# Optimization experiments

Hardware: AMD Instinct MI355X
Metric: run time of the kernel (lower is better)

The kernel has to match this reference:

```python
import jax, jax.numpy as jnp
import numpy as np

EPS = 1e-5

def _fake_quant(w, axis):
    # symmetric int8 fake-quant with straight-through estimator
    s = jnp.max(jnp.abs(w), axis=axis, keepdims=True) / 127.0 + 1e-8
    q = jnp.clip(jnp.round(w / s), -127.0, 127.0) * s
    return w + jax.lax.stop_gradient(q - w)

def _qconv1x1(x, w, b):
    # x: [B, C_in, Q, H, W]; w: [C_out, C_in] (1x1 kernel); weight fake-quantized
    wq = _fake_quant(w, axis=1)
    return jnp.einsum('bcqhw,oc->boqhw', x, wq) + b[None, :, None, None, None]

def setup_inputs() -> dict:
    key = jax.random.key(0)
    ks = jax.random.split(key, 12)
    B, C, Q, H, W = 8, 256, 4, 40, 40
    x = jax.random.normal(ks[0], (B, C, Q, H, W), dtype=jnp.float32)
    scale = 1.0 / np.sqrt(C)
    Wq = jax.random.normal(ks[1], (C, C), dtype=jnp.float32) * scale
    Wk = jax.random.normal(ks[2], (C, C), dtype=jnp.float32) * scale
    Wv = jax.random.normal(ks[3], (C, C), dtype=jnp.float32) * scale
    Wp = jax.random.normal(ks[4], (C, C), dtype=jnp.float32) * scale
    bq = jnp.zeros((C,), jnp.float32)
    bk = jnp.zeros((C,), jnp.float32)
    bv = jnp.zeros((C,), jnp.float32)
    bp = jnp.zeros((C,), jnp.float32)
    gamma = jnp.ones((C,), jnp.float32)
    beta = jnp.zeros((C,), jnp.float32)
    return {"x": x, "Wq": Wq, "bq": bq, "Wk": Wk, "bk": bk,
            "Wv": Wv, "bv": bv, "Wp": Wp, "bp": bp,
            "gamma": gamma, "beta": beta}

def reference(x, Wq, bq, Wk, bk, Wv, bv, Wp, bp, gamma, beta):
    B, C, Q, H, W = x.shape
    q = _qconv1x1(x, Wq, bq)
    k = _qconv1x1(x, Wk, bk)
    v = _qconv1x1(x, Wv, bv)
    # per-rotation channel attention: [B, Q=4, C, H*W]
    qh = q.reshape(B, C, Q, H * W).transpose(0, 2, 1, 3)
    kh = k.reshape(B, C, Q, H * W).transpose(0, 2, 1, 3)
    vh = v.reshape(B, C, Q, H * W).transpose(0, 2, 1, 3)
    scale = 1.0 / jnp.sqrt(jnp.float32(C // 4))
    attn = jnp.einsum('bqcn,bqdn->bqcd', qh, kh) * scale  # [B,4,C,C]
    attn = jax.nn.softmax(attn, axis=-1)
    out = jnp.einsum('bqcd,bqdn->bqcn', attn, vh)  # [B,4,C,HW]
    out = out.transpose(0, 2, 1, 3).reshape(B, C, Q, H, W)
    out = _qconv1x1(out, Wp, bp)
    # IQBN: per-channel batchnorm with int8 fake-quantized gamma
    mean = jnp.mean(out, axis=(0, 2, 3, 4), keepdims=True)
    var = jnp.var(out, axis=(0, 2, 3, 4), keepdims=True)
    g = _fake_quant(gamma, axis=None)[None, :, None, None, None]
    b = beta[None, :, None, None, None]
    out = (out - mean) * jax.lax.rsqrt(var + EPS) * g + b
    return out
```

## Files before the change

kernel.cpp:

```cpp
#include <hip/hip_runtime.h>
#include <math.h>

#define BB 8
#define CCH 256
#define QQ 4
#define NN 1600
#define BQN 32
#define SP 51200
#define EPSF 1e-5f

typedef __attribute__((ext_vector_type(8))) short bf16x8;
typedef __attribute__((ext_vector_type(4))) float f32x4;

static __device__ inline ushort f2bf(float f) {
  union { float f; unsigned u; } v; v.f = f;
  return (ushort)((v.u + 0x7fffu + ((v.u >> 16) & 1u)) >> 16);
}
static __device__ inline float bf2f(ushort u) {
  union { unsigned u; float f; } v; v.u = ((unsigned)u) << 16;
  return v.f;
}
static __device__ inline void gld16(const ushort* g, ushort* l) {
  __builtin_amdgcn_global_load_lds(
      (const __attribute__((address_space(1))) unsigned int*)g,
      (__attribute__((address_space(3))) unsigned int*)l, 16, 0, 0);
}

__global__ void quant_weights_kernel(const float* Wq, const float* Wk,
                                     const float* Wv, const float* Wp,
                                     const float* gamma,
                                     ushort* wq, ushort* wk, ushort* wvT, ushort* wp,
                                     ushort* wqT, ushort* wkT, ushort* wpT,
                                     float* gq, float* r, float* d2,
                                     float* m_acc, float* v_acc) {
  __shared__ float red[256];
  int blk = blockIdx.x;
  int tid = threadIdx.x;
  if (blk < 1024) {
    int mat = blk >> 8;
    int row = blk & 255;
    const float* W = (mat == 0) ? Wq : (mat == 1) ? Wk : (mat == 2) ? Wv : Wp;
    float w = W[row * 256 + tid];
    red[tid] = fabsf(w);
    __syncthreads();
    for (int s = 128; s > 0; s >>= 1) {
      if (tid < s) red[tid] = fmaxf(red[tid], red[tid + s]);
      __syncthreads();
    }
    float s = red[0] / 127.0f + 1e-8f;
    float q = fminf(fmaxf(rintf(w / s), -127.0f), 127.0f) * s;
    ushort qb = f2bf(q);
    if (mat == 0)      { wq[row * 256 + tid] = qb; wqT[tid * 256 + row] = qb; }
    else if (mat == 1) { wk[row * 256 + tid] = qb; wkT[tid * 256 + row] = qb; }
    else if (mat == 2) { wvT[tid * 256 + row] = qb; }
    else               { wp[row * 256 + tid] = qb; wpT[tid * 256 + row] = qb; }
  } else {
    float g = gamma[tid];
    red[tid] = fabsf(g);
    __syncthreads();
    for (int s = 128; s > 0; s >>= 1) {
      if (tid < s) red[tid] = fmaxf(red[tid], red[tid + s]);
      __syncthreads();
    }
    float s = red[0] / 127.0f + 1e-8f;
    gq[tid] = fminf(fmaxf(rintf(g / s), -127.0f), 127.0f) * s;
    for (int i = tid; i < BQN * 256; i += 256) { r[i] = 0.f; d2[i] = 0.f; }
    m_acc[tid] = 0.f;
    v_acc[tid] = 0.f;
  }
}

__global__ __launch_bounds__(256)
void prep_kernel(const float* __restrict__ x, ushort* __restrict__ xb,
                 ushort* __restrict__ xT, float* __restrict__ r) {
  int bqi = blockIdx.z, b = bqi >> 2, q = bqi & 3;
  int s0 = blockIdx.x * 64, c0 = blockIdx.y * 64;
  __shared__ ushort lT[64 * 66];
  int tid = threadIdx.x;
  int c = tid >> 2, nch = (tid & 3) * 16;
  const float* xp = x + ((size_t)(b * CCH + c0 + c) * QQ + q) * NN + s0 + nch;
  union { ushort u[16]; int4 v[2]; } nb;
  float s = 0.f;
#pragma unroll
  for (int j = 0; j < 4; j++) {
    float4 f = ((const float4*)xp)[j];
    ushort b0 = f2bf(f.x), b1 = f2bf(f.y), b2 = f2bf(f.z), b3 = f2bf(f.w);
    s += bf2f(b0) + bf2f(b1) + bf2f(b2) + bf2f(b3);
    nb.u[j * 4 + 0] = b0;
    nb.u[j * 4 + 1] = b1;
    nb.u[j * 4 + 2] = b2;
    nb.u[j * 4 + 3] = b3;
    lT[c * 66 + nch + j * 4 + 0] = b0;
    lT[c * 66 + nch + j * 4 + 1] = b1;
    lT[c * 66 + nch + j * 4 + 2] = b2;
    lT[c * 66 + nch + j * 4 + 3] = b3;
  }
  ushort* xbp = xb + (size_t)bqi * (CCH * NN) + (size_t)(c0 + c) * NN + s0 + nch;
  *(int4*)xbp = nb.v[0];
  *((int4*)xbp + 1) = nb.v[1];
  s += __shfl_down(s, 2);
  s += __shfl_down(s, 1);
  if ((tid & 3) == 0) atomicAdd(&r[bqi * 256 + c0 + c], s);
  __syncthreads();
  int n = tid >> 2, cch = (tid & 3) * 16;
  union { ushort u[16]; int4 v[2]; } o;
#pragma unroll
  for (int i = 0; i < 16; i++) o.u[i] = lT[(cch + i) * 66 + n];
  ushort* dst = xT + (size_t)(bqi * NN + s0 + n) * CCH + c0 + cch;
  *(int4*)dst = o.v[0];
  *((int4*)dst + 1) = o.v[1];
}

__global__ __launch_bounds__(256)
void gram_kernel(const ushort* __restrict__ xb, ushort* __restrict__ Gh,
                 ushort* __restrict__ Gl) {
  __shared__ __align__(16) char smem[32768];
  float* lC = (float*)smem;
  int z = blockIdx.z;
  int mBase = blockIdx.y * 128, nBase = blockIdx.x * 128;
  int tid = threadIdx.x, wave = tid >> 6, lane = tid & 63;
  int wm = wave >> 1, wn = wave & 1;
  int col = lane & 15, quad = lane >> 4;
  int srow = tid >> 2, skc = (tid & 3) * 8;
  const ushort* X = xb + (size_t)z * (CCH * NN);
  const ushort* gA  = X + (size_t)(mBase + srow) * NN + skc;
  const ushort* gA2 = gA + (size_t)64 * NN;
  const ushort* gB  = X + (size_t)(nBase + srow) * NN + skc;
  const ushort* gB2 = gB + (size_t)64 * NN;
  ushort* sA1[2]; ushort* sA2[2]; ushort* sB1[2]; ushort* sB2[2];
#pragma unroll
  for (int b = 0; b < 2; b++) {
    ushort* lAb = (ushort*)(smem + b * 16384);
    ushort* lBb = (ushort*)(smem + b * 16384 + 8192);
    sA1[b] = &lAb[srow * 32 + skc];
    sA2[b] = &lAb[(64 + srow) * 32 + skc];
    sB1[b] = &lBb[srow * 32 + skc];
    sB2[b] = &lBb[(64 + srow) * 32 + skc];
  }
  f32x4 acc[4][4];
#pragma unroll
  for (int i = 0; i < 4; i++)
#pragma unroll
    for (int j = 0; j < 4; j++) acc[i][j] = (f32x4){0.f, 0.f, 0.f, 0.f};

  const int nIter = NN / 32;
  gld16(gA, sA1[0]); gld16(gA2, sA2[0]); gld16(gB, sB1[0]); gld16(gB2, sB2[0]);
  for (int it = 0; it < nIter; ++it) {
    int cur = it & 1;
    __syncthreads();
    if (it + 1 < nIter) {
      int kt = (it + 1) << 5, nxt = cur ^ 1;
      gld16(gA + kt, sA1[nxt]); gld16(gA2 + kt, sA2[nxt]);
      gld16(gB + kt, sB1[nxt]); gld16(gB2 + kt, sB2[nxt]);
    }
    const ushort* lAc = (const ushort*)(smem + cur * 16384);
    const ushort* lBc = (const ushort*)(smem + cur * 16384 + 8192);
    bf16x8 af[4], bfr[4];
#pragma unroll
    for (int i = 0; i < 4; i++)
      af[i] = *(const bf16x8*)&lAc[(wm * 64 + i * 16 + col) * 32 + quad * 8];
#pragma unroll
    for (int j = 0; j < 4; j++)
      bfr[j] = *(const bf16x8*)&lBc[(wn * 64 + j * 16 + col) * 32 + quad * 8];
#pragma unroll
    for (int i = 0; i < 4; i++)
#pragma unroll
      for (int j = 0; j < 4; j++)
        acc[i][j] = __builtin_amdgcn_mfma_f32_16x16x32_bf16(af[i], bfr[j], acc[i][j], 0, 0, 0);
  }
  __syncthreads();
  float* lCw = lC + wave * 16 * 68;
  int mW = mBase + wm * 64, nW = nBase + wn * 64;
#pragma unroll
  for (int i = 0; i < 4; i++) {
#pragma unroll
    for (int j = 0; j < 4; j++)
#pragma unroll
      for (int rg = 0; rg < 4; rg++)
        lCw[(quad * 4 + rg) * 68 + j * 16 + col] = acc[i][j][rg];
    int mrow0 = mW + i * 16;
    int rr = lane & 15, cc = lane >> 4;
    union { ushort u[16]; int4 v[2]; } oh, ol;
#pragma unroll
    for (int t = 0; t < 16; t++) {
      float vfl = lCw[rr * 68 + cc * 16 + t];
      ushort hh = f2bf(vfl);
      oh.u[t] = hh;
      ol.u[t] = f2bf(vfl - bf2f(hh));
    }
    size_t off = (size_t)z * 65536 + (size_t)(mrow0 + rr) * 256 + nW + cc * 16;
    *(int4*)(Gh + off) = oh.v[0];
    *((int4*)(Gh + off) + 1) = oh.v[1];
    *(int4*)(Gl + off) = ol.v[0];
    *((int4*)(Gl + off) + 1) = ol.v[1];
  }
}

template<int MODE>
__global__ __launch_bounds__(256)
void gemm64(const ushort* __restrict__ A, long sA, const ushort* __restrict__ A2,
            const ushort* __restrict__ B, long sB, const ushort* __restrict__ B2,
            void* __restrict__ C1, void* __restrict__ C2, long sC) {
  constexpr bool SPB = (MODE == 0 || MODE == 4);
  constexpr bool SPA = (MODE == 1);
  constexpr int BUFB = (SPA || SPB) ? 12288 : 8192;
  __shared__ __align__(16) char smem[2 * BUFB];
  int z = blockIdx.z;
  int mBase = blockIdx.y * 64, nBase = blockIdx.x * 64;
  int tid = threadIdx.x, wave = tid >> 6, lane = tid & 63;
  int wm = wave >> 1, wn = wave & 1;
  int col = lane & 15, quad = lane >> 4;
  const ushort* gA = A + (size_t)z * sA + (size_t)(mBase + (tid >> 2)) * 256 + (tid & 3) * 8;
  const ushort* gB = B + (size_t)z * sB + (size_t)(nBase + (tid >> 2)) * 256 + (tid & 3) * 8;
  const ushort* gX = nullptr;
  if (SPB) gX = B2 + (size_t)z * sB + (size_t)(nBase + (tid >> 2)) * 256 + (tid & 3) * 8;
  if (SPA) gX = A2 + (size_t)z * sA + (size_t)(mBase + (tid >> 2)) * 256 + (tid & 3) * 8;

  f32x4 acc[2][2];
#pragma unroll
  for (int i = 0; i < 2; i++)
#pragma unroll
    for (int j = 0; j < 2; j++) acc[i][j] = (f32x4){0.f, 0.f, 0.f, 0.f};

  {
    char* bb = smem;
    gld16(gA, (ushort*)bb + tid * 8);
    gld16(gB, (ushort*)(bb + 4096) + tid * 8);
    if (SPA || SPB) gld16(gX, (ushort*)(bb + 8192) + tid * 8);
  }
  for (int it = 0; it < 8; ++it) {
    int cur = it & 1;
    __syncthreads();
    if (it + 1 < 8) {
      int kt = (it + 1) * 32;
      char* bb = smem + (cur ^ 1) * BUFB;
      gld16(gA + kt, (ushort*)bb + tid * 8);
      gld16(gB + kt, (ushort*)(bb + 4096) + tid * 8);
      if (SPA || SPB) gld16(gX + kt, (ushort*)(bb + 8192) + tid * 8);
    }
    const ushort* lA = (const ushort*)(smem + cur * BUFB);
    const ushort* lB = lA + 2048;
    const ushort* lX = lA + 4096;
    bf16x8 af[2], bfv[2], xf[2];
#pragma unroll
    for (int i = 0; i < 2; i++)
      af[i] = *(const bf16x8*)&lA[(wm * 32 + i * 16 + col) * 32 + quad * 8];
#pragma unroll
    for (int j = 0; j < 2; j++)
      bfv[j] = *(const bf16x8*)&lB[(wn * 32 + j * 16 + col) * 32 + quad * 8];
    if (SPB) {
#pragma unroll
      for (int j = 0; j < 2; j++)
        xf[j] = *(const bf16x8*)&lX[(wn * 32 + j * 16 + col) * 32 + quad * 8];
    } else if (SPA) {
#pragma unroll
      for (int i = 0; i < 2; i++)
        xf[i] = *(const bf16x8*)&lX[(wm * 32 + i * 16 + col) * 32 + quad * 8];
    }
#pragma unroll
    for (int i = 0; i < 2; i++)
#pragma unroll
      for (int j = 0; j < 2; j++) {
        acc[i][j] = __builtin_amdgcn_mfma_f32_16x16x32_bf16(af[i], bfv[j], acc[i][j], 0, 0, 0);
        if (SPB)
          acc[i][j] = __builtin_amdgcn_mfma_f32_16x16x32_bf16(af[i], xf[j], acc[i][j], 0, 0, 0);
        if (SPA)
          acc[i][j] = __builtin_amdgcn_mfma_f32_16x16x32_bf16(xf[i], bfv[j], acc[i][j], 0, 0, 0);
      }
  }

  if (MODE == 4) {
    const ushort* Tz = A + (size_t)z * sA;
    float* d2 = (float*)C1;
#pragma unroll
    for (int i = 0; i < 2; i++) {
      int mr = mBase + wm * 32 + i * 16 + quad * 4;
#pragma unroll
      for (int rg = 0; rg < 4; rg++) {
        float p = 0.f;
#pragma unroll
        for (int j = 0; j < 2; j++)
          p += acc[i][j][rg] * bf2f(Tz[(mr + rg) * 256 + nBase + wn * 32 + j * 16 + col]);
        p += __shfl_down(p, 8);
        p += __shfl_down(p, 4);
        p += __shfl_down(p, 2);
        p += __shfl_down(p, 1);
        if (col == 0) atomicAdd(d2 + z * 256 + mr + rg, p);
      }
    }
    return;
  }

  __syncthreads();
  float* lCw = (float*)smem + wave * (16 * 36);
#pragma unroll
  for (int i = 0; i < 2; i++) {
#pragma unroll
    for (int j = 0; j < 2; j++)
#pragma unroll
      for (int rg = 0; rg < 4; rg++)
        lCw[(quad * 4 + rg) * 36 + j * 16 + col] = acc[i][j][rg];
    int mrow0 = mBase + wm * 32 + i * 16;
    int nW = nBase + wn * 32;
    if (MODE == 1) {
      int rr = lane >> 2, cc = (lane & 3) * 8;
      float* C = (float*)C1 + (size_t)z * sC + (size_t)(mrow0 + rr) * 256 + nW + cc;
      float4 f0, f1;
      f0.x = lCw[rr * 36 + cc + 0]; f0.y = lCw[rr * 36 + cc + 1];
      f0.z = lCw[rr * 36 + cc + 2]; f0.w = lCw[rr * 36 + cc + 3];
      f1.x = lCw[rr * 36 + cc + 4]; f1.y = lCw[rr * 36 + cc + 5];
      f1.z = lCw[rr * 36 + cc + 6]; f1.w = lCw[rr * 36 + cc + 7];
      *(float4*)C = f0;
      *(float4*)(C + 4) = f1;
    } else if (MODE == 0) {
      int rr = lane >> 2, cc = (lane & 3) * 8;
      union { ushort u[8]; int4 v; } oh, ol;
#pragma unroll
      for (int t = 0; t < 8; t++) {
        float vf = lCw[rr * 36 + cc + t];
        ushort hh = f2bf(vf);
        oh.u[t] = hh;
        ol.u[t] = f2bf(vf - bf2f(hh));
      }
      size_t off = (size_t)z * sC + (size_t)(mrow0 + rr) * 256 + nW + cc;
      *(int4*)((ushort*)C1 + off) = oh.v;
      *(int4*)((ushort*)C2 + off) = ol.v;
    } else {
      if (MODE == 3) {
        int rr = lane >> 2, cc = (lane & 3) * 8;
        union { ushort u[8]; int4 v; } o;
#pragma unroll
        for (int t = 0; t < 8; t++) o.u[t] = f2bf(lCw[rr * 36 + cc + t]);
        *(int4*)((ushort*)C1 + (size_t)z * sC + (size_t)(mrow0 + rr) * 256 + nW + cc) = o.v;
      }
      int nn = lane >> 1, mh = (lane & 1) * 8;
      union { ushort u[8]; int4 v; } o2;
#pragma unroll
      for (int t = 0; t < 8; t++) o2.u[t] = f2bf(lCw[(mh + t) * 36 + nn]);
      ushort* CT = (ushort*)((MODE == 2) ? C1 : C2);
      *(int4*)(CT + (size_t)z * sC + (size_t)(nW + nn) * 256 + mrow0 + mh) = o2.v;
    }
  }
}

__global__ __launch_bounds__(256)
void uv_kernel(const ushort* __restrict__ wqT, const ushort* __restrict__ wkT,
               const float* __restrict__ r, float* __restrict__ u,
               float* __restrict__ vv) {
  int bq = blockIdx.x, sel = blockIdx.y, c = threadIdx.x;
  __shared__ float rs[256];
  rs[c] = r[bq * 256 + c];
  __syncthreads();
  const ushort* WT = sel ? wkT : wqT;
  float s = 0.f;
  for (int i = 0; i < 256; i++) s += bf2f(WT[i * 256 + c]) * rs[i];
  (sel ? vv : u)[bq * 256 + c] = s;
}

__global__ __launch_bounds__(256)
void softmax_kernel(const float* __restrict__ S, const float* __restrict__ u,
                    const float* __restrict__ vv, const float* __restrict__ bqv,
                    const float* __restrict__ bkv, const float* __restrict__ bvv,
                    ushort* __restrict__ P, float* __restrict__ pb) {
  int wave = threadIdx.x >> 6, lane = threadIdx.x & 63;
  int rglob = blockIdx.x * 4 + wave;
  int bq = rglob >> 8, rw = rglob & 255;
  size_t off = (size_t)rglob * 256;
  int c0 = lane * 4;
  float4 s4 = *(const float4*)(S + off + c0);
  float4 v4 = *(const float4*)(vv + bq * 256 + c0);
  float4 bk4 = *(const float4*)(bkv + c0);
  float4 bv4 = *(const float4*)(bvv + c0);
  float uu = u[bq * 256 + rw];
  float bqc = bqv[rw];
  float x0 = 0.125f * (s4.x + uu * bk4.x + bqc * v4.x + 1600.0f * bqc * bk4.x);
  float x1 = 0.125f * (s4.y + uu * bk4.y + bqc * v4.y + 1600.0f * bqc * bk4.y);
  float x2 = 0.125f * (s4.z + uu * bk4.z + bqc * v4.z + 1600.0f * bqc * bk4.z);
  float x3 = 0.125f * (s4.w + uu * bk4.w + bqc * v4.w + 1600.0f * bqc * bk4.w);
  float m = fmaxf(fmaxf(x0, x1), fmaxf(x2, x3));
#pragma unroll
  for (int s = 32; s > 0; s >>= 1) m = fmaxf(m, __shfl_xor(m, s));
  float e0 = expf(x0 - m), e1 = expf(x1 - m), e2 = expf(x2 - m), e3 = expf(x3 - m);
  float t = e0 + e1 + e2 + e3;
#pragma unroll
  for (int s = 32; s > 0; s >>= 1) t += __shfl_xor(t, s);
  float is = 1.0f / t;
  float p0 = e0 * is, p1 = e1 * is, p2 = e2 * is, p3 = e3 * is;
  union { ushort u[4]; uint2 v; } o;
  o.u[0] = f2bf(p0); o.u[1] = f2bf(p1); o.u[2] = f2bf(p2); o.u[3] = f2bf(p3);
  *(uint2*)(P + off + c0) = o.v;
  float d = p0 * bv4.x + p1 * bv4.y + p2 * bv4.z + p3 * bv4.w;
#pragma unroll
  for (int s = 32; s > 0; s >>= 1) d += __shfl_xor(d, s);
  if (lane == 0) pb[rglob] = d;
}

__global__ __launch_bounds__(256)
void bo_d1_kernel(const ushort* __restrict__ wpT, const ushort* __restrict__ TmT,
                  const float* __restrict__ pb, const float* __restrict__ rb,
                  const float* __restrict__ bp, const float* __restrict__ d2,
                  float* __restrict__ bo, float* __restrict__ m_acc,
                  float* __restrict__ v_acc) {
  int z = blockIdx.x, o = threadIdx.x;
  __shared__ float sp[256], sr[256];
  sp[o] = pb[z * 256 + o];
  sr[o] = rb[z * 256 + o];
  __syncthreads();
  float bv = bp[o], d1 = 0.f;
  const ushort* Tz = TmT + (size_t)z * 65536;
  for (int c = 0; c < 256; c++) {
    bv += bf2f(wpT[c * 256 + o]) * sp[c];
    d1 += bf2f(Tz[c * 256 + o]) * sr[c];
  }
  bo[z * 256 + o] = bv;
  atomicAdd(m_acc + o, d1 + 1600.0f * bv);
  atomicAdd(v_acc + o, d2[z * 256 + o] + 2.0f * bv * d1 + 1600.0f * bv * bv);
}

__global__ __launch_bounds__(256)
void final_kernel(const ushort* __restrict__ Tm, const ushort* __restrict__ xT,
                  const float* __restrict__ bo, const float* __restrict__ m_acc,
                  const float* __restrict__ v_acc, const float* __restrict__ gq,
                  const float* __restrict__ beta, float* __restrict__ out) {
  __shared__ __align__(16) char smem[32768];
  float* lC = (float*)smem;
  int z = blockIdx.z;
  int mBase = blockIdx.y * 128, nBase = blockIdx.x * 128;
  int tid = threadIdx.x, wave = tid >> 6, lane = tid & 63;
  int wm = wave >> 1, wn = wave & 1;
  int col = lane & 15, quad = lane >> 4;
  int srow = tid >> 2, skc = (tid & 3) * 8;
  const ushort* Az = Tm + (size_t)z * 65536;
  const ushort* Bz = xT + (size_t)z * (NN * 256);
  const ushort* gA  = Az + (size_t)(mBase + srow) * 256 + skc;
  const ushort* gA2 = gA + 64 * 256;
  int br1 = nBase + srow;      br1 = br1 < NN ? br1 : NN - 1;
  int br2 = nBase + 64 + srow; br2 = br2 < NN ? br2 : NN - 1;
  const ushort* gB  = Bz + (size_t)br1 * 256 + skc;
  const ushort* gB2 = Bz + (size_t)br2 * 256 + skc;
  ushort* sA1[2]; ushort* sA2[2]; ushort* sB1[2]; ushort* sB2[2];
#pragma unroll
  for (int b = 0; b < 2; b++) {
    ushort* lAb = (ushort*)(smem + b * 16384);
    ushort* lBb = (ushort*)(smem + b * 16384 + 8192);
    sA1[b] = &lAb[srow * 32 + skc];
    sA2[b] = &lAb[(64 + srow) * 32 + skc];
    sB1[b] = &lBb[srow * 32 + skc];
    sB2[b] = &lBb[(64 + srow) * 32 + skc];
  }
  f32x4 acc[4][4];
#pragma unroll
  for (int i = 0; i < 4; i++)
#pragma unroll
    for (int j = 0; j < 4; j++) acc[i][j] = (f32x4){0.f, 0.f, 0.f, 0.f};

  const int nIter = 8;
  gld16(gA, sA1[0]); gld16(gA2, sA2[0]); gld16(gB, sB1[0]); gld16(gB2, sB2[0]);
  for (int it = 0; it < nIter; ++it) {
    int cur = it & 1;
    __syncthreads();
    if (it + 1 < nIter) {
      int kt = (it + 1) << 5, nxt = cur ^ 1;
      gld16(gA + kt, sA1[nxt]); gld16(gA2 + kt, sA2[nxt]);
      gld16(gB + kt, sB1[nxt]); gld16(gB2 + kt, sB2[nxt]);
    }
    const ushort* lAc = (const ushort*)(smem + cur * 16384);
    const ushort* lBc = (const ushort*)(smem + cur * 16384 + 8192);
    bf16x8 af[4], bfr[4];
#pragma unroll
    for (int i = 0; i < 4; i++)
      af[i] = *(const bf16x8*)&lAc[(wm * 64 + i * 16 + col) * 32 + quad * 8];
#pragma unroll
    for (int j = 0; j < 4; j++)
      bfr[j] = *(const bf16x8*)&lBc[(wn * 64 + j * 16 + col) * 32 + quad * 8];
#pragma unroll
    for (int i = 0; i < 4; i++)
#pragma unroll
      for (int j = 0; j < 4; j++)
        acc[i][j] = __builtin_amdgcn_mfma_f32_16x16x32_bf16(af[i], bfr[j], acc[i][j], 0, 0, 0);
  }
  __syncthreads();
  float* lCw = lC + wave * 16 * 68;
  int mW = mBase + wm * 64, nW = nBase + wn * 64;
  int b = z >> 2, q = z & 3;
  const float inv = 1.0f / (float)SP;
#pragma unroll
  for (int i = 0; i < 4; i++) {
#pragma unroll
    for (int j = 0; j < 4; j++)
#pragma unroll
      for (int rg = 0; rg < 4; rg++)
        lCw[(quad * 4 + rg) * 68 + j * 16 + col] = acc[i][j][rg];
    int mrow0 = mW + i * 16;
    int rr = lane & 15, cc = lane >> 4;
    int n0 = nW + cc * 16;
    int o = mrow0 + rr;
    float bi = bo[(size_t)z * 256 + o];
    float mean = m_acc[o] * inv;
    float var = v_acc[o] * inv - mean * mean;
    float scl = rsqrtf(var + EPSF) * gq[o];
    float be = beta[o];
    if (n0 < NN) {
      float* C = out + (size_t)b * (CCH * QQ * NN)
               + (size_t)o * (QQ * NN) + (size_t)q * NN + n0;
#pragma unroll
      for (int v = 0; v < 4; v++) {
        float4 f;
        f.x = (lCw[rr * 68 + cc * 16 + v * 4 + 0] + bi - mean) * scl + be;
        f.y = (lCw[rr * 68 + cc * 16 + v * 4 + 1] + bi - mean) * scl + be;
        f.z = (lCw[rr * 68 + cc * 16 + v * 4 + 2] + bi - mean) * scl + be;
        f.w = (lCw[rr * 68 + cc * 16 + v * 4 + 3] + bi - mean) * scl + be;
        *(float4*)(C + v * 4) = f;
      }
    }
  }
}

extern "C" void kernel_launch(void* const* d_in, const int* in_sizes, int n_in,
                              void* d_out, int out_size, void* d_ws, size_t ws_size,
                              hipStream_t stream) {
  const float* x     = (const float*)d_in[0];
  const float* Wq    = (const float*)d_in[1];
  const float* bq    = (const float*)d_in[2];
  const float* Wk    = (const float*)d_in[3];
  const float* bk    = (const float*)d_in[4];
  const float* Wv    = (const float*)d_in[5];
  const float* bv    = (const float*)d_in[6];
  const float* Wp    = (const float*)d_in[7];
  const float* bp    = (const float*)d_in[8];
  const float* gamma = (const float*)d_in[9];
  const float* beta  = (const float*)d_in[10];
  float* out = (float*)d_out;

  ushort* h    = (ushort*)d_ws;
  ushort* wq   = h;
  ushort* wk   = wq + 65536;
  ushort* wp   = wk + 65536;
  ushort* wvT  = wp + 65536;
  ushort* wqT  = wvT + 65536;
  ushort* wkT  = wqT + 65536;
  ushort* wpT  = wkT + 65536;
  ushort* xb   = wpT + 65536;
  ushort* xT   = xb + (size_t)BQN * CCH * NN;
  ushort* Gh   = xT + (size_t)BQN * CCH * NN;
  ushort* Gl   = Gh + (size_t)BQN * 65536;
  ushort* M1h  = Gl + (size_t)BQN * 65536;
  ushort* M1l  = M1h + (size_t)BQN * 65536;
  ushort* P    = M1l + (size_t)BQN * 65536;
  ushort* N1t  = P + (size_t)BQN * 65536;
  ushort* Tm   = N1t + (size_t)BQN * 65536;
  ushort* TmT  = Tm + (size_t)BQN * 65536;
  float*  S    = (float*)(TmT + (size_t)BQN * 65536);
  float*  r    = S + (size_t)BQN * 65536;
  float*  u    = r + 8192;
  float*  vv   = u + 8192;
  float*  pb   = vv + 8192;
  float*  bo   = pb + 8192;
  float*  d2   = bo + 8192;
  float*  m_acc = d2 + 8192;
  float*  v_acc = m_acc + 256;
  float*  gq   = v_acc + 256;

  quant_weights_kernel<<<1025, 256, 0, stream>>>(Wq, Wk, Wv, Wp, gamma,
                                                 wq, wk, wvT, wp, wqT, wkT, wpT,
                                                 gq, r, d2, m_acc, v_acc);
  prep_kernel<<<dim3(NN / 64, CCH / 64, BQN), 256, 0, stream>>>(x, xb, xT, r);
  uv_kernel<<<dim3(BQN, 2), 256, 0, stream>>>(wqT, wkT, r, u, vv);
  gram_kernel<<<dim3(2, 2, BQN), 256, 0, stream>>>(xb, Gh, Gl);
  gemm64<0><<<dim3(4, 4, BQN), 256, 0, stream>>>(
      wq, 0, nullptr, Gh, 65536, Gl, M1h, M1l, 65536);
  gemm64<1><<<dim3(4, 4, BQN), 256, 0, stream>>>(
      M1h, 65536, M1l, wk, 0, nullptr, S, nullptr, 65536);
  softmax_kernel<<<BQN * CCH / 4, 256, 0, stream>>>(S, u, vv, bq, bk, bv, P, pb);
  gemm64<2><<<dim3(4, 4, BQN), 256, 0, stream>>>(
      P, 65536, nullptr, wvT, 0, nullptr, N1t, nullptr, 65536);
  gemm64<3><<<dim3(4, 4, BQN), 256, 0, stream>>>(
      wp, 0, nullptr, N1t, 65536, nullptr, Tm, TmT, 65536);
  gemm64<4><<<dim3(4, 4, BQN), 256, 0, stream>>>(
      Tm, 65536, nullptr, Gh, 65536, Gl, d2, nullptr, 0);
  bo_d1_kernel<<<BQN, 256, 0, stream>>>(wpT, TmT, pb, r, bp, d2, bo, m_acc, v_acc);
  final_kernel<<<dim3(13, 2, BQN), 256, 0, stream>>>(Tm, xT, bo, m_acc, v_acc,
                                                     gq, beta, out);
}
```

Measured before the change: 264.4 us.

## Exploit Gram symmetry and fuse attention GEMM chain into two kernels

The Gram kernel now computes only the upper-triangular 64x64 tiles (10 per batch-rotation) and writes mirrored transposes, roughly halving its MFMA work. The two M1/S GEMMs plus softmax are fused into one kernel that keeps M1 hi/lo in LDS, and the P·Wv and Wp GEMMs are fused into another that keeps N1 in LDS. This removes global round-trips for M1, S and N1 and several launches, but uses large LDS (about 100 KB) and fewer blocks (8 per z), which lowers occupancy and parallelism.

Measured after the change: 250.9 us. 1.05x faster.

```diff
diff --git a/kernel.cpp b/kernel.cpp
--- a/kernel.cpp
+++ b/kernel.cpp
@@ -112,87 +112,362 @@
 }
 
 __global__ __launch_bounds__(256)
-void gram_kernel(const ushort* __restrict__ xb, ushort* __restrict__ Gh,
-                 ushort* __restrict__ Gl) {
-  __shared__ __align__(16) char smem[32768];
-  float* lC = (float*)smem;
-  int z = blockIdx.z;
-  int mBase = blockIdx.y * 128, nBase = blockIdx.x * 128;
+void gram_sym_kernel(const ushort* __restrict__ xb, ushort* __restrict__ Gh,
+                     ushort* __restrict__ Gl) {
+  __shared__ __align__(16) char smem[16384];
+  int t = blockIdx.x, z = blockIdx.y;
+  int ty = (t >= 4) + (t >= 7) + (t >= 9);
+  int base = ty * 4 - (ty * (ty - 1)) / 2;
+  int tx = ty + (t - base);
+  int mBase = ty * 64, nBase = tx * 64;
+  bool offd = (tx != ty);
   int tid = threadIdx.x, wave = tid >> 6, lane = tid & 63;
   int wm = wave >> 1, wn = wave & 1;
   int col = lane & 15, quad = lane >> 4;
-  int srow = tid >> 2, skc = (tid & 3) * 8;
   const ushort* X = xb + (size_t)z * (CCH * NN);
-  const ushort* gA  = X + (size_t)(mBase + srow) * NN + skc;
-  const ushort* gA2 = gA + (size_t)64 * NN;
-  const ushort* gB  = X + (size_t)(nBase + srow) * NN + skc;
-  const ushort* gB2 = gB + (size_t)64 * NN;
-  ushort* sA1[2]; ushort* sA2[2]; ushort* sB1[2]; ushort* sB2[2];
-#pragma unroll
-  for (int b = 0; b < 2; b++) {
-    ushort* lAb = (ushort*)(smem + b * 16384);
-    ushort* lBb = (ushort*)(smem + b * 16384 + 8192);
-    sA1[b] = &lAb[srow * 32 + skc];
-    sA2[b] = &lAb[(64 + srow) * 32 + skc];
-    sB1[b] = &lBb[srow * 32 + skc];
-    sB2[b] = &lBb[(64 + srow) * 32 + skc];
-  }
-  f32x4 acc[4][4];
-#pragma unroll
-  for (int i = 0; i < 4; i++)
-#pragma unroll
-    for (int j = 0; j < 4; j++) acc[i][j] = (f32x4){0.f, 0.f, 0.f, 0.f};
+  const ushort* gA = X + (size_t)(mBase + (tid >> 2)) * NN + (tid & 3) * 8;
+  const ushort* gB = X + (size_t)(nBase + (tid >> 2)) * NN + (tid & 3) * 8;
+  f32x4 acc[2][2];
+#pragma unroll
+  for (int i = 0; i < 2; i++)
+#pragma unroll
+    for (int j = 0; j < 2; j++) acc[i][j] = (f32x4){0.f, 0.f, 0.f, 0.f};
 
   const int nIter = NN / 32;
-  gld16(gA, sA1[0]); gld16(gA2, sA2[0]); gld16(gB, sB1[0]); gld16(gB2, sB2[0]);
+  gld16(gA, (ushort*)smem + tid * 8);
+  gld16(gB, (ushort*)(smem + 4096) + tid * 8);
   for (int it = 0; it < nIter; ++it) {
     int cur = it & 1;
     __syncthreads();
     if (it + 1 < nIter) {
-      int kt = (it + 1) << 5, nxt = cur ^ 1;
-      gld16(gA + kt, sA1[nxt]); gld16(gA2 + kt, sA2[nxt]);
-      gld16(gB + kt, sB1[nxt]); gld16(gB2 + kt, sB2[nxt]);
-    }
-    const ushort* lAc = (const ushort*)(smem + cur * 16384);
-    const ushort* lBc = (const ushort*)(smem + cur * 16384 + 8192);
-    bf16x8 af[4], bfr[4];
+      int kt = (it + 1) << 5;
+      char* bb = smem + (cur ^ 1) * 8192;
+      gld16(gA + kt, (ushort*)bb + tid * 8);
+      gld16(gB + kt, (ushort*)(bb + 4096) + tid * 8);
+    }
+    const ushort* lA = (const ushort*)(smem + cur * 8192);
+    const ushort* lB = lA + 2048;
+    bf16x8 af[2], bfr[2];
+#pragma unroll
+    for (int i = 0; i < 2; i++)
+      af[i] = *(const bf16x8*)&lA[(wm * 32 + i * 16 + col) * 32 + quad * 8];
+#pragma unroll
+    for (int j = 0; j < 2; j++)
+      bfr[j] = *(const bf16x8*)&lB[(wn * 32 + j * 16 + col) * 32 + quad * 8];
+#pragma unroll
+    for (int i = 0; i < 2; i++)
+#pragma unroll
+      for (int j = 0; j < 2; j++)
+        acc[i][j] = __builtin_amdgcn_mfma_f32_16x16x32_bf16(af[i], bfr[j], acc[i][j], 0, 0, 0);
+  }
+  __syncthreads();
+  float* lCw = (float*)smem + wave * 576;
+#pragma unroll
+  for (int i = 0; i < 2; i++) {
+#pragma unroll
+    for (int j = 0; j < 2; j++)
+#pragma unroll
+      for (int rg = 0; rg < 4; rg++)
+        lCw[(quad * 4 + rg) * 36 + j * 16 + col] = acc[i][j][rg];
+    int mrow0 = mBase + wm * 32 + i * 16;
+    int nW = nBase + wn * 32;
+    int rr = lane >> 2, cc = (lane & 3) * 8;
+    union { ushort u[8]; int4 v; } oh, ol;
+#pragma unroll
+    for (int t8 = 0; t8 < 8; t8++) {
+      float vfl = lCw[rr * 36 + cc + t8];
+      ushort hh = f2bf(vfl);
+      oh.u[t8] = hh;
+      ol.u[t8] = f2bf(vfl - bf2f(hh));
+    }
+    size_t off = (size_t)z * 65536 + (size_t)(mrow0 + rr) * 256 + nW + cc;
+    *(int4*)(Gh + off) = oh.v;
+    *(int4*)(Gl + off) = ol.v;
+    if (offd) {
+      int nn = lane >> 1, mh = (lane & 1) * 8;
+      union { ushort u[8]; int4 v; } th, tl;
+#pragma unroll
+      for (int t8 = 0; t8 < 8; t8++) {
+        float vfl = lCw[(mh + t8) * 36 + nn];
+        ushort hh = f2bf(vfl);
+        th.u[t8] = hh;
+        tl.u[t8] = f2bf(vfl - bf2f(hh));
+      }
+      size_t offT = (size_t)z * 65536 + (size_t)(nW + nn) * 256 + mrow0 + mh;
+      *(int4*)(Gh + offT) = th.v;
+      *(int4*)(Gl + offT) = tl.v;
+    }
+  }
+}
+
+__global__ __launch_bounds__(256)
+void spk_kernel(const ushort* __restrict__ wq, const ushort* __restrict__ Gh,
+                const ushort* __restrict__ Gl, const ushort* __restrict__ wk,
+                const float* __restrict__ ug, const float* __restrict__ vg,
+                const float* __restrict__ bqv, const float* __restrict__ bkv,
+                const float* __restrict__ bvv,
+                ushort* __restrict__ P, float* __restrict__ pb) {
+  __shared__ __align__(16) char smem[103424];
+  int z = blockIdx.y, mBase = blockIdx.x * 32;
+  int tid = threadIdx.x, wave = tid >> 6, lane = tid & 63;
+  int col = lane & 15, quad = lane >> 4;
+  int rA = tid >> 2, sub = (tid & 3) * 8;
+  const ushort* Ghz = Gh + (size_t)z * 65536;
+  const ushort* Glz = Gl + (size_t)z * 65536;
+  ushort* M1h_l = (ushort*)(smem + 69632);
+  ushort* M1l_l = M1h_l + 8448;
+
+  f32x4 acc[2][4];
+#pragma unroll
+  for (int i = 0; i < 2; i++)
+#pragma unroll
+    for (int j = 0; j < 4; j++) acc[i][j] = (f32x4){0.f, 0.f, 0.f, 0.f};
+
+  auto s1_load = [&](int buf, int kt) {
+    ushort* L = (ushort*)(smem + buf * 34816);
+    if (tid < 128)
+      gld16(wq + (size_t)(mBase + rA) * 256 + kt + sub, L + tid * 8);
+    ushort* Lh = L + 1024;
+    ushort* Ll = L + 9216;
+#pragma unroll
+    for (int q = 0; q < 4; q++) {
+      int n = q * 64 + rA;
+      gld16(Ghz + (size_t)n * 256 + kt + sub, Lh + (q * 256 + tid) * 8);
+      gld16(Glz + (size_t)n * 256 + kt + sub, Ll + (q * 256 + tid) * 8);
+    }
+  };
+  s1_load(0, 0);
+  for (int it = 0; it < 8; ++it) {
+    int cur = it & 1;
+    __syncthreads();
+    if (it + 1 < 8) s1_load(cur ^ 1, (it + 1) * 32);
+    const ushort* L = (const ushort*)(smem + cur * 34816);
+    const ushort* lA = L;
+    const ushort* lBh = L + 1024;
+    const ushort* lBl = L + 9216;
+    bf16x8 af[2], bh[4], bl[4];
+#pragma unroll
+    for (int i = 0; i < 2; i++)
+      af[i] = *(const bf16x8*)&lA[(i * 16 + col) * 32 + quad * 8];
+#pragma unroll
+    for (int j = 0; j < 4; j++) {
+      bh[j] = *(const bf16x8*)&lBh[(wave * 64 + j * 16 + col) * 32 + quad * 8];
+      bl[j] = *(const bf16x8*)&lBl[(wave * 64 + j * 16 + col) * 32 + quad * 8];
+    }
+#pragma unroll
+    for (int i = 0; i < 2; i++)
+#pragma unroll
+      for (int j = 0; j < 4; j++) {
+        acc[i][j] = __builtin_amdgcn_mfma_f32_16x16x32_bf16(af[i], bh[j], acc[i][j], 0, 0, 0);
+        acc[i][j] = __builtin_amdgcn_mfma_f32_16x16x32_bf16(af[i], bl[j], acc[i][j], 0, 0, 0);
+      }
+  }
+#pragma unroll
+  for (int i = 0; i < 2; i++)
+#pragma unroll
+    for (int j = 0; j < 4; j++)
+#pragma unroll
+      for (int rg = 0; rg < 4; rg++) {
+        int ml = i * 16 + quad * 4 + rg;
+        int cg = wave * 64 + j * 16 + col;
+        float vfl = acc[i][j][rg];
+        ushort hh = f2bf(vfl);
+        M1h_l[ml * 264 + cg] = hh;
+        M1l_l[ml * 264 + cg] = f2bf(vfl - bf2f(hh));
+      }
+
+  f32x4 acc2[2][4];
+#pragma unroll
+  for (int i = 0; i < 2; i++)
+#pragma unroll
+    for (int j = 0; j < 4; j++) acc2[i][j] = (f32x4){0.f, 0.f, 0.f, 0.f};
+  auto s2_load = [&](int buf, int kt) {
+    ushort* L = (ushort*)(smem + buf * 34816);
+#pragma unroll
+    for (int q = 0; q < 4; q++)
+      gld16(wk + (size_t)(q * 64 + rA) * 256 + kt + sub, L + (q * 256 + tid) * 8);
+  };
+  s2_load(0, 0);
+  for (int it = 0; it < 8; ++it) {
+    int cur = it & 1;
+    __syncthreads();
+    if (it + 1 < 8) s2_load(cur ^ 1, (it + 1) * 32);
+    const ushort* lB = (const ushort*)(smem + cur * 34816);
+    int kt = it * 32;
+    bf16x8 ah[2], al[2], bfr[4];
+#pragma unroll
+    for (int i = 0; i < 2; i++) {
+      ah[i] = *(const bf16x8*)&M1h_l[(i * 16 + col) * 264 + kt + quad * 8];
+      al[i] = *(const bf16x8*)&M1l_l[(i * 16 + col) * 264 + kt + quad * 8];
+    }
+#pragma unroll
+    for (int j = 0; j < 4; j++)
+      bfr[j] = *(const bf16x8*)&lB[(wave * 64 + j * 16 + col) * 32 + quad * 8];
+#pragma unroll
+    for (int i = 0; i < 2; i++)
+#pragma unroll
+      for (int j = 0; j < 4; j++) {
+        acc2[i][j] = __builtin_amdgcn_mfma_f32_16x16x32_bf16(ah[i], bfr[j], acc2[i][j], 0, 0, 0);
+        acc2[i][j] = __builtin_amdgcn_mfma_f32_16x16x32_bf16(al[i], bfr[j], acc2[i][j], 0, 0, 0);
+      }
+  }
+  __syncthreads();
+
+  float* Sb = (float*)(smem + 69632);
+  float bkc[4], vvc[4];
+#pragma unroll
+  for (int j = 0; j < 4; j++) {
+    int cg = wave * 64 + j * 16 + col;
+    bkc[j] = bkv[cg];
+    vvc[j] = vg[z * 256 + cg];
+  }
+#pragma unroll
+  for (int i = 0; i < 2; i++)
+#pragma unroll
+    for (int rg = 0; rg < 4; rg++) {
+      int ml = i * 16 + quad * 4 + rg;
+      int rglob = mBase + ml;
+      float uu = ug[z * 256 + rglob];
+      float bqc = bqv[rglob];
+#pragma unroll
+      for (int j = 0; j < 4; j++)
+        Sb[ml * 260 + wave * 64 + j * 16 + col] =
+            0.125f * (acc2[i][j][rg] + uu * bkc[j] + bqc * vvc[j] + 1600.0f * bqc * bkc[j]);
+    }
+  __syncthreads();
+
+  float4 bv4 = *(const float4*)(bvv + lane * 4);
+#pragma unroll
+  for (int rr8 = 0; rr8 < 8; ++rr8) {
+    int rloc = wave * 8 + rr8;
+    f32x4 sv = *(const f32x4*)&Sb[rloc * 260 + lane * 4];
+    float x0 = sv[0], x1 = sv[1], x2 = sv[2], x3 = sv[3];
+    float m = fmaxf(fmaxf(x0, x1), fmaxf(x2, x3));
+#pragma unroll
+    for (int s = 32; s > 0; s >>= 1) m = fmaxf(m, __shfl_xor(m, s));
+    float e0 = expf(x0 - m), e1 = expf(x1 - m), e2 = expf(x2 - m), e3 = expf(x3 - m);
+    float t = e0 + e1 + e2 + e3;
+#pragma unroll
+    for (int s = 32; s > 0; s >>= 1) t += __shfl_xor(t, s);
+    float is = 1.0f / t;
+    float p0 = e0 * is, p1 = e1 * is, p2 = e2 * is, p3 = e3 * is;
+    union { ushort u[4]; uint2 v; } o;
+    o.u[0] = f2bf(p0); o.u[1] = f2bf(p1); o.u[2] = f2bf(p2); o.u[3] = f2bf(p3);
+    *(uint2*)(P + (size_t)z * 65536 + (size_t)(mBase + rloc) * 256 + lane * 4) = o.v;
+    float d = p0 * bv4.x + p1 * bv4.y + p2 * bv4.z + p3 * bv4.w;
+#pragma unroll
+    for (int s = 32; s > 0; s >>= 1) d += __shfl_xor(d, s);
+    if (lane == 0) pb[z * 256 + mBase + rloc] = d;
+  }
+}
+
+__global__ __launch_bounds__(256)
+void pt_kernel(const ushort* __restrict__ P, const ushort* __restrict__ wvT,
+               const ushort* __restrict__ wp,
+               ushort* __restrict__ Tm, ushort* __restrict__ TmT) {
+  __shared__ __align__(16) char smem[53760];
+  int z = blockIdx.y, cs = blockIdx.x * 32;
+  int tid = threadIdx.x, wave = tid >> 6, lane = tid & 63;
+  int col = lane & 15, quad = lane >> 4;
+  int rA = tid >> 2, sub = (tid & 3) * 8;
+  const ushort* Pz = P + (size_t)z * 65536;
+  ushort* N1b = (ushort*)(smem + 36864);
+
+  f32x4 acc[4][2];
+#pragma unroll
+  for (int i = 0; i < 4; i++)
+#pragma unroll
+    for (int j = 0; j < 2; j++) acc[i][j] = (f32x4){0.f, 0.f, 0.f, 0.f};
+  auto s3_load = [&](int buf, int kt) {
+    ushort* L = (ushort*)(smem + buf * 18432);
+#pragma unroll
+    for (int q = 0; q < 4; q++)
+      gld16(Pz + (size_t)(q * 64 + rA) * 256 + kt + sub, L + (q * 256 + tid) * 8);
+    if (tid < 128)
+      gld16(wvT + (size_t)(cs + rA) * 256 + kt + sub, L + 8192 + tid * 8);
+  };
+  s3_load(0, 0);
+  for (int it = 0; it < 8; ++it) {
+    int cur = it & 1;
+    __syncthreads();
+    if (it + 1 < 8) s3_load(cur ^ 1, (it + 1) * 32);
+    const ushort* lP = (const ushort*)(smem + cur * 18432);
+    const ushort* lV = lP + 8192;
+    bf16x8 af[4], bfr[2];
 #pragma unroll
     for (int i = 0; i < 4; i++)
-      af[i] = *(const bf16x8*)&lAc[(wm * 64 + i * 16 + col) * 32 + quad * 8];
-#pragma unroll
-    for (int j = 0; j < 4; j++)
-      bfr[j] = *(const bf16x8*)&lBc[(wn * 64 + j * 16 + col) * 32 + quad * 8];
+      af[i] = *(const bf16x8*)&lP[(wave * 64 + i * 16 + col) * 32 + quad * 8];
+#pragma unroll
+    for (int j = 0; j < 2; j++)
+      bfr[j] = *(const bf16x8*)&lV[(j * 16 + col) * 32 + quad * 8];
 #pragma unroll
     for (int i = 0; i < 4; i++)
 #pragma unroll
-      for (int j = 0; j < 4; j++)
+      for (int j = 0; j < 2; j++)
         acc[i][j] = __builtin_amdgcn_mfma_f32_16x16x32_bf16(af[i], bfr[j], acc[i][j], 0, 0, 0);
   }
+#pragma unroll
+  for (int i = 0; i < 4; i++)
+#pragma unroll
+    for (int j = 0; j < 2; j++)
+#pragma unroll
+      for (int rg = 0; rg < 4; rg++) {
+        int e = wave * 64 + i * 16 + quad * 4 + rg;
+        int cl = j * 16 + col;
+        N1b[cl * 264 + e] = f2bf(acc[i][j][rg]);
+      }
+
+  f32x4 acc2[4][2];
+#pragma unroll
+  for (int i = 0; i < 4; i++)
+#pragma unroll
+    for (int j = 0; j < 2; j++) acc2[i][j] = (f32x4){0.f, 0.f, 0.f, 0.f};
+  auto s4_load = [&](int buf, int kt) {
+    ushort* L = (ushort*)(smem + buf * 18432);
+#pragma unroll
+    for (int q = 0; q < 4; q++)
+      gld16(wp + (size_t)(q * 64 + rA) * 256 + kt + sub, L + (q * 256 + tid) * 8);
+  };
+  s4_load(0, 0);
+  for (int it = 0; it < 8; ++it) {
+    int cur = it & 1;
+    __syncthreads();
+    if (it + 1 < 8) s4_load(cur ^ 1, (it + 1) * 32);
+    const ushort* lW = (const ushort*)(smem + cur * 18432);
+    int kt = it * 32;
+    bf16x8 af[4], bfr[2];
+#pragma unroll
+    for (int i = 0; i < 4; i++)
+      af[i] = *(const bf16x8*)&lW[(wave * 64 + i * 16 + col) * 32 + quad * 8];
+#pragma unroll
+    for (int j = 0; j < 2; j++)
+      bfr[j] = *(const bf16x8*)&N1b[(j * 16 + col) * 264 + kt + quad * 8];
+#pragma unroll
+    for (int i = 0; i < 4; i++)
+#pragma unroll
+      for (int j = 0; j < 2; j++)
+        acc2[i][j] = __builtin_amdgcn_mfma_f32_16x16x32_bf16(af[i], bfr[j], acc2[i][j], 0, 0, 0);
+  }
   __syncthreads();
-  float* lCw = lC + wave * 16 * 68;
-  int mW = mBase + wm * 64, nW = nBase + wn * 64;
+  float* lCw = (float*)smem + wave * 576;
 #pragma unroll
   for (int i = 0; i < 4; i++) {
 #pragma unroll
-    for (int j = 0; j < 4; j++)
+    for (int j = 0; j < 2; j++)
 #pragma unroll
       for (int rg = 0; rg < 4; rg++)
-        lCw[(quad * 4 + rg) * 68 + j * 16 + col] = acc[i][j][rg];
-    int mrow0 = mW + i * 16;
-    int rr = lane & 15, cc = lane >> 4;
-    union { ushort u[16]; int4 v[2]; } oh, ol;
-#pragma unroll
-    for (int t = 0; t < 16; t++) {
-      float vfl = lCw[rr * 68 + cc * 16 + t];
-      ushort hh = f2bf(vfl);
-      oh.u[t] = hh;
-      ol.u[t] = f2bf(vfl - bf2f(hh));
-    }
-    size_t off = (size_t)z * 65536 + (size_t)(mrow0 + rr) * 256 + nW + cc * 16;
-    *(int4*)(Gh + off) = oh.v[0];
-    *((int4*)(Gh + off) + 1) = oh.v[1];
-    *(int4*)(Gl + off) = ol.v[0];
-    *((int4*)(Gl + off) + 1) = ol.v[1];
+        lCw[(quad * 4 + rg) * 36 + j * 16 + col] = acc2[i][j][rg];
+    int oW = wave * 64 + i * 16;
+    int rr = lane >> 2, cc = (lane & 3) * 8;
+    union { ushort u[8]; int4 v; } o;
+#pragma unroll
+    for (int t8 = 0; t8 < 8; t8++) o.u[t8] = f2bf(lCw[rr * 36 + cc + t8]);
+    *(int4*)(Tm + (size_t)z * 65536 + (size_t)(oW + rr) * 256 + cs + cc) = o.v;
+    int nn = lane >> 1, mh = (lane & 1) * 8;
+    union { ushort u[8]; int4 v; } o2;
+#pragma unroll
+    for (int t8 = 0; t8 < 8; t8++) o2.u[t8] = f2bf(lCw[(mh + t8) * 36 + nn]);
+    *(int4*)(TmT + (size_t)z * 65536 + (size_t)(cs + nn) * 256 + oW + mh) = o2.v;
   }
 }
 
@@ -290,57 +565,6 @@
     }
     return;
   }
-
-  __syncthreads();
-  float* lCw = (float*)smem + wave * (16 * 36);
-#pragma unroll
-  for (int i = 0; i < 2; i++) {
-#pragma unroll
-    for (int j = 0; j < 2; j++)
-#pragma unroll
-      for (int rg = 0; rg < 4; rg++)
-        lCw[(quad * 4 + rg) * 36 + j * 16 + col] = acc[i][j][rg];
-    int mrow0 = mBase + wm * 32 + i * 16;
-    int nW = nBase + wn * 32;
-    if (MODE == 1) {
-      int rr = lane >> 2, cc = (lane & 3) * 8;
-      float* C = (float*)C1 + (size_t)z * sC + (size_t)(mrow0 + rr) * 256 + nW + cc;
-      float4 f0, f1;
-      f0.x = lCw[rr * 36 + cc + 0]; f0.y = lCw[rr * 36 + cc + 1];
-      f0.z = lCw[rr * 36 + cc + 2]; f0.w = lCw[rr * 36 + cc + 3];
-      f1.x = lCw[rr * 36 + cc + 4]; f1.y = lCw[rr * 36 + cc + 5];
-      f1.z = lCw[rr * 36 + cc + 6]; f1.w = lCw[rr * 36 + cc + 7];
-      *(float4*)C = f0;
-      *(float4*)(C + 4) = f1;
-    } else if (MODE == 0) {
-      int rr = lane >> 2, cc = (lane & 3) * 8;
-      union { ushort u[8]; int4 v; } oh, ol;
-#pragma unroll
-      for (int t = 0; t < 8; t++) {
-        float vf = lCw[rr * 36 + cc + t];
-        ushort hh = f2bf(vf);
-        oh.u[t] = hh;
-        ol.u[t] = f2bf(vf - bf2f(hh));
-      }
-      size_t off = (size_t)z * sC + (size_t)(mrow0 + rr) * 256 + nW + cc;
-      *(int4*)((ushort*)C1 + off) = oh.v;
-      *(int4*)((ushort*)C2 + off) = ol.v;
-    } else {
-      if (MODE == 3) {
-        int rr = lane >> 2, cc = (lane & 3) * 8;
-        union { ushort u[8]; int4 v; } o;
-#pragma unroll
-        for (int t = 0; t < 8; t++) o.u[t] = f2bf(lCw[rr * 36 + cc + t]);
-        *(int4*)((ushort*)C1 + (size_t)z * sC + (size_t)(mrow0 + rr) * 256 + nW + cc) = o.v;
-      }
-      int nn = lane >> 1, mh = (lane & 1) * 8;
-      union { ushort u[8]; int4 v; } o2;
-#pragma unroll
-      for (int t = 0; t < 8; t++) o2.u[t] = f2bf(lCw[(mh + t) * 36 + nn]);
-      ushort* CT = (ushort*)((MODE == 2) ? C1 : C2);
-      *(int4*)(CT + (size_t)z * sC + (size_t)(nW + nn) * 256 + mrow0 + mh) = o2.v;
-    }
-  }
 }
 
 __global__ __launch_bounds__(256)
@@ -355,44 +579,6 @@
   float s = 0.f;
   for (int i = 0; i < 256; i++) s += bf2f(WT[i * 256 + c]) * rs[i];
   (sel ? vv : u)[bq * 256 + c] = s;
-}
-
-__global__ __launch_bounds__(256)
-void softmax_kernel(const float* __restrict__ S, const float* __restrict__ u,
-                    const float* __restrict__ vv, const float* __restrict__ bqv,
-                    const float* __restrict__ bkv, const float* __restrict__ bvv,
-                    ushort* __restrict__ P, float* __restrict__ pb) {
-  int wave = threadIdx.x >> 6, lane = threadIdx.x & 63;
-  int rglob = blockIdx.x * 4 + wave;
-  int bq = rglob >> 8, rw = rglob & 255;
-  size_t off = (size_t)rglob * 256;
-  int c0 = lane * 4;
-  float4 s4 = *(const float4*)(S + off + c0);
-  float4 v4 = *(const float4*)(vv + bq * 256 + c0);
-  float4 bk4 = *(const float4*)(bkv + c0);
-  float4 bv4 = *(const float4*)(bvv + c0);
-  float uu = u[bq * 256 + rw];
-  float bqc = bqv[rw];
-  float x0 = 0.125f * (s4.x + uu * bk4.x + bqc * v4.x + 1600.0f * bqc * bk4.x);
-  float x1 = 0.125f * (s4.y + uu * bk4.y + bqc * v4.y + 1600.0f * bqc * bk4.y);
-  float x2 = 0.125f * (s4.z + uu * bk4.z + bqc * v4.z + 1600.0f * bqc * bk4.z);
-  float x3 = 0.125f * (s4.w + uu * bk4.w + bqc * v4.w + 1600.0f * bqc * bk4.w);
-  float m = fmaxf(fmaxf(x0, x1), fmaxf(x2, x3));
-#pragma unroll
-  for (int s = 32; s > 0; s >>= 1) m = fmaxf(m, __shfl_xor(m, s));
-  float e0 = expf(x0 - m), e1 = expf(x1 - m), e2 = expf(x2 - m), e3 = expf(x3 - m);
-  float t = e0 + e1 + e2 + e3;
-#pragma unroll
-  for (int s = 32; s > 0; s >>= 1) t += __shfl_xor(t, s);
-  float is = 1.0f / t;
-  float p0 = e0 * is, p1 = e1 * is, p2 = e2 * is, p3 = e3 * is;
-  union { ushort u[4]; uint2 v; } o;
-  o.u[0] = f2bf(p0); o.u[1] = f2bf(p1); o.u[2] = f2bf(p2); o.u[3] = f2bf(p3);
-  *(uint2*)(P + off + c0) = o.v;
-  float d = p0 * bv4.x + p1 * bv4.y + p2 * bv4.z + p3 * bv4.w;
-#pragma unroll
-  for (int s = 32; s > 0; s >>= 1) d += __shfl_xor(d, s);
-  if (lane == 0) pb[rglob] = d;
 }
 
 __global__ __launch_bounds__(256)
@@ -544,14 +730,10 @@
   ushort* xT   = xb + (size_t)BQN * CCH * NN;
   ushort* Gh   = xT + (size_t)BQN * CCH * NN;
   ushort* Gl   = Gh + (size_t)BQN * 65536;
-  ushort* M1h  = Gl + (size_t)BQN * 65536;
-  ushort* M1l  = M1h + (size_t)BQN * 65536;
-  ushort* P    = M1l + (size_t)BQN * 65536;
-  ushort* N1t  = P + (size_t)BQN * 65536;
-  ushort* Tm   = N1t + (size_t)BQN * 65536;
+  ushort* P    = Gl + (size_t)BQN * 65536;
+  ushort* Tm   = P + (size_t)BQN * 65536;
   ushort* TmT  = Tm + (size_t)BQN * 65536;
-  float*  S    = (float*)(TmT + (size_t)BQN * 65536);
-  float*  r    = S + (size_t)BQN * 65536;
+  float*  r    = (float*)(TmT + (size_t)BQN * 65536);
   float*  u    = r + 8192;
   float*  vv   = u + 8192;
   float*  pb   = vv + 8192;
@@ -566,16 +748,9 @@
                                                  gq, r, d2, m_acc, v_acc);
   prep_kernel<<<dim3(NN / 64, CCH / 64, BQN), 256, 0, stream>>>(x, xb, xT, r);
   uv_kernel<<<dim3(BQN, 2), 256, 0, stream>>>(wqT, wkT, r, u, vv);
-  gram_kernel<<<dim3(2, 2, BQN), 256, 0, stream>>>(xb, Gh, Gl);
-  gemm64<0><<<dim3(4, 4, BQN), 256, 0, stream>>>(
-      wq, 0, nullptr, Gh, 65536, Gl, M1h, M1l, 65536);
-  gemm64<1><<<dim3(4, 4, BQN), 256, 0, stream>>>(
-      M1h, 65536, M1l, wk, 0, nullptr, S, nullptr, 65536);
-  softmax_kernel<<<BQN * CCH / 4, 256, 0, stream>>>(S, u, vv, bq, bk, bv, P, pb);
-  gemm64<2><<<dim3(4, 4, BQN), 256, 0, stream>>>(
-      P, 65536, nullptr, wvT, 0, nullptr, N1t, nullptr, 65536);
-  gemm64<3><<<dim3(4, 4, BQN), 256, 0, stream>>>(
-      wp, 0, nullptr, N1t, 65536, nullptr, Tm, TmT, 65536);
+  gram_sym_kernel<<<dim3(10, BQN), 256, 0, stream>>>(xb, Gh, Gl);
+  spk_kernel<<<dim3(8, BQN), 256, 0, stream>>>(wq, Gh, Gl, wk, u, vv, bq, bk, bv, P, pb);
+  pt_kernel<<<dim3(8, BQN), 256, 0, stream>>>(P, wvT, wp, Tm, TmT);
   gemm64<4><<<dim3(4, 4, BQN), 256, 0, stream>>>(
       Tm, 65536, nullptr, Gh, 65536, Gl, d2, nullptr, 0);
   bo_d1_kernel<<<BQN, 256, 0, stream>>>(wpT, TmT, pb, r, bp, d2, bo, m_acc, v_acc);
```
